# Kernel tuning notes

Measured on AMD Instinct MI355X. Metric: run time of the kernel, lower is better.

The kernel has to match this reference:

```python
import jax, jax.numpy as jnp
import numpy as np

B, S, DIM, HEADS, EXPERTS = 2, 2048, 1024, 16, 8
DFF = 4 * DIM
EPS = 1e-5


def setup_inputs() -> dict:
    key = jax.random.key(0)
    ks = jax.random.split(key, 16)
    w = lambda k, shp: jax.random.normal(k, shp, dtype=jnp.float32) * 0.02
    return {
        "x": jax.random.normal(ks[0], (B, S, DIM), dtype=jnp.float32),
        "ln1_g": jnp.ones((DIM,), jnp.float32), "ln1_b": jnp.zeros((DIM,), jnp.float32),
        "ln2_g": jnp.ones((DIM,), jnp.float32), "ln2_b": jnp.zeros((DIM,), jnp.float32),
        "wq": w(ks[1], (DIM, DIM)), "bq": jnp.zeros((DIM,), jnp.float32),
        "wk": w(ks[2], (DIM, DIM)), "bk": jnp.zeros((DIM,), jnp.float32),
        "wv": w(ks[3], (DIM, DIM)), "bv": jnp.zeros((DIM,), jnp.float32),
        "wo": w(ks[4], (DIM, DIM)), "bo": jnp.zeros((DIM,), jnp.float32),
        "w1": w(ks[5], (EXPERTS, DIM, DFF)), "b1": jnp.zeros((EXPERTS, DFF), jnp.float32),
        "w2": w(ks[6], (EXPERTS, DFF, DIM)), "b2": jnp.zeros((EXPERTS, DIM), jnp.float32),
        "token_split": np.full(EXPERTS, S // EXPERTS, dtype=np.int64),  # static split sizes
        "heads": HEADS,
    }


def _layernorm(h, g, b):
    m = h.mean(-1, keepdims=True)
    v = ((h - m) ** 2).mean(-1, keepdims=True)
    return (h - m) * jax.lax.rsqrt(v + EPS) * g + b


def reference(x, ln1_g, ln1_b, ln2_g, ln2_b, wq, bq, wk, bk, wv, bv, wo, bo,
              w1, b1, w2, b2, token_split, heads):
    Bx, Sx, D = x.shape
    Dh = D // heads
    # --- attention on norm1(x) ---
    h = _layernorm(x, ln1_g, ln1_b)
    q = (h @ wq + bq).reshape(Bx, Sx, heads, Dh)
    k = (h @ wk + bk).reshape(Bx, Sx, heads, Dh)
    v = (h @ wv + bv).reshape(Bx, Sx, heads, Dh)
    scores = jnp.einsum('bqhd,bkhd->bhqk', q, k) * (Dh ** -0.5)
    attn = jax.nn.softmax(scores, axis=-1)
    o = jnp.einsum('bhqk,bkhd->bqhd', attn, v).reshape(Bx, Sx, D)
    x = x + (o @ wo + bo)
    # --- token-chunked per-expert MLP ---
    residual = x
    h = _layernorm(x, ln2_g, ln2_b)
    split_pts = np.cumsum(np.asarray(token_split))[:-1]  # static boundaries
    chunks = jnp.split(h, split_pts, axis=1)
    outs = [jax.nn.silu(c @ w1[e] + b1[e]) @ w2[e] + b2[e]
            for e, c in enumerate(chunks)]
    return jnp.concatenate(outs, axis=1) + residual
```

## Files before the change

kernel.cpp:

```cpp
#include <hip/hip_runtime.h>


typedef unsigned int  u32;
typedef unsigned short u16;
typedef short v8s __attribute__((ext_vector_type(8)));
typedef float v4f __attribute__((ext_vector_type(4)));

#define SEQ  2048
#define DIM_ 1024
#define EPS_ 1e-5f

__device__ __forceinline__ u16 f2bf(float f) {
    __bf16 h = (__bf16)f;
    return __builtin_bit_cast(u16, h);
}

__device__ __forceinline__ void gload16(const void* g, void* l) {
    __builtin_amdgcn_global_load_lds((const __attribute__((address_space(1))) u32*)g,
                                     (__attribute__((address_space(3))) u32*)l, 16, 0, 0);
}

template<bool SEP>
__global__ __launch_bounds__(256) void conv_t(const float* __restrict__ s0,
                                              const float* __restrict__ s1,
                                              const float* __restrict__ s2,
                                              const float* __restrict__ s3,
                                              u16* __restrict__ dst, int K, int N) {
    __shared__ __attribute__((aligned(16))) u16 Ts[64][72];
    int tid = threadIdx.x;
    int z = blockIdx.z;
    const float* src = SEP ? (z == 0 ? s0 : z == 1 ? s1 : z == 2 ? s2 : s3)
                           : s0 + (size_t)z * K * N;
    u16* d = dst + (size_t)z * K * N;
    int k0 = blockIdx.y * 64, n0 = blockIdx.x * 64;
    int tk = tid >> 4, tn = tid & 15;

    u16 t[4][4];
    #pragma unroll
    for (int r = 0; r < 4; r++) {
        float4 L = *(const float4*)&src[(size_t)(k0 + tk * 4 + r) * N + n0 + tn * 4];
        t[r][0] = f2bf(L.x); t[r][1] = f2bf(L.y); t[r][2] = f2bf(L.z); t[r][3] = f2bf(L.w);
    }
    #pragma unroll
    for (int c = 0; c < 4; c++) {
        ushort4 q4 = { t[0][c], t[1][c], t[2][c], t[3][c] };
        *(ushort4*)&Ts[tn * 4 + c][tk * 4] = q4;
    }
    __syncthreads();
    #pragma unroll
    for (int i = 0; i < 2; i++) {
        int id = tid + i * 256;
        int row = id >> 3, ch = id & 7;
        v8s val = *(const v8s*)&Ts[row][ch * 8];
        *(v8s*)&d[(size_t)(n0 + row) * K + k0 + ch * 8] = val;
    }
}

__global__ __launch_bounds__(256) void ln_kernel(const float* __restrict__ x,
                                                 const float* __restrict__ g,
                                                 const float* __restrict__ b,
                                                 u16* __restrict__ out) {
    int row = blockIdx.x;
    int t = threadIdx.x;
    const float4* xr = (const float4*)(x + (size_t)row * DIM_);
    float4 v = xr[t];
    float s  = v.x + v.y + v.z + v.w;
    float ss = v.x*v.x + v.y*v.y + v.z*v.z + v.w*v.w;
    #pragma unroll
    for (int off = 32; off > 0; off >>= 1) {
        s  += __shfl_down(s, off);
        ss += __shfl_down(ss, off);
    }
    __shared__ float red[8];
    if ((t & 63) == 0) { red[t >> 6] = s; red[4 + (t >> 6)] = ss; }
    __syncthreads();
    s  = red[0] + red[1] + red[2] + red[3];
    ss = red[4] + red[5] + red[6] + red[7];
    float mean = s * (1.0f / DIM_);
    float var  = ss * (1.0f / DIM_) - mean * mean;
    float rstd = rsqrtf(var + EPS_);
    float4 gv = ((const float4*)g)[t];
    float4 bv = ((const float4*)b)[t];
    ushort4 ov;
    ov.x = f2bf((v.x - mean) * rstd * gv.x + bv.x);
    ov.y = f2bf((v.y - mean) * rstd * gv.y + bv.y);
    ov.z = f2bf((v.z - mean) * rstd * gv.z + bv.z);
    ov.w = f2bf((v.w - mean) * rstd * gv.w + bv.w);
    *(ushort4*)(out + (size_t)row * DIM_ + t * 4) = ov;
}

template<int BN, int ACT, bool GROUPED, int WMODE>
__global__ __launch_bounds__(256) void gemm_bf16(
    const u16* __restrict__ A, const u16* __restrict__ WT,
    const float* __restrict__ b0, const float* __restrict__ bk2, const float* __restrict__ bv2,
    const float* __restrict__ resid, float* __restrict__ Cf,
    u16* __restrict__ Cb, u16* __restrict__ Ckb, u16* __restrict__ vtb,
    int Nw, int K)
{
    constexpr int BM = 128;
    constexpr int MI = 4;
    constexpr int NI = BN / 32;
    __shared__ __attribute__((aligned(16))) char AsB[BM * 128];
    __shared__ __attribute__((aligned(16))) char BsB[BN * 128];

    int tid = threadIdx.x;
    int lane = tid & 63, w = tid >> 6;
    int wr = w >> 1, wc = w & 1;
    int g = lane >> 4, lq = lane & 15;

    long row0; int e = 0;
    const float* bias = b0;
    if (GROUPED) {
        int seg = blockIdx.y >> 1, mh = blockIdx.y & 1;
        int bb = seg >> 3; e = seg & 7;
        row0 = (long)bb * SEQ + e * 256 + mh * BM;
        bias += (size_t)e * Nw;
    } else row0 = (long)blockIdx.y * BM;

    int col0 = blockIdx.x * BN;
    int colL = col0;
    if (WMODE == 2) {
        int sel = col0 >> 10; colL = col0 & 1023;
        if (sel == 1)      bias = bk2;
        else if (sel == 2) bias = bv2;
    }

    const u16* Arow = A + (size_t)row0 * K;
    const u16* Brow = WT + (GROUPED ? ((size_t)e * Nw + col0) : (size_t)col0) * K;

    v4f acc[MI][NI];
    #pragma unroll
    for (int mi = 0; mi < MI; mi++)
        #pragma unroll
        for (int ni = 0; ni < NI; ni++) acc[mi][ni] = (v4f){0.f, 0.f, 0.f, 0.f};

    for (int kt = 0; kt < K; kt += 64) {
        #pragma unroll
        for (int i = 0; i < 4; i++) {
            int R0 = (i * 4 + w) * 8;
            int row = R0 + (lane >> 3);
            gload16(Arow + (size_t)row * K + kt + (((lane & 7) ^ (row & 7)) << 3),
                    AsB + R0 * 128);
        }
        #pragma unroll
        for (int i = 0; i < NI; i++) {
            int R0 = (i * 4 + w) * 8;
            int row = R0 + (lane >> 3);
            gload16(Brow + (size_t)row * K + kt + (((lane & 7) ^ (row & 7)) << 3),
                    BsB + R0 * 128);
        }
        __syncthreads();
        #pragma unroll
        for (int kk = 0; kk < 64; kk += 32) {
            v8s af[MI], bfv[NI];
            int slot = (kk >> 3) + g;
            #pragma unroll
            for (int mi = 0; mi < MI; mi++) {
                int row = wr * 64 + mi * 16 + lq;
                af[mi] = *(const v8s*)(AsB + row * 128 + ((slot ^ (row & 7)) << 4));
            }
            #pragma unroll
            for (int ni = 0; ni < NI; ni++) {
                int rn = wc * (BN / 2) + ni * 16 + lq;
                bfv[ni] = *(const v8s*)(BsB + rn * 128 + ((slot ^ (rn & 7)) << 4));
            }
            #pragma unroll
            for (int mi = 0; mi < MI; mi++)
                #pragma unroll
                for (int ni = 0; ni < NI; ni++)
                    acc[mi][ni] = __builtin_amdgcn_mfma_f32_16x16x32_bf16(
                        af[mi], bfv[ni], acc[mi][ni], 0, 0, 0);
        }
        __syncthreads();
    }

    #pragma unroll
    for (int mi = 0; mi < MI; mi++) {
        int grow = wr * 64 + mi * 16 + g * 4;
        #pragma unroll
        for (int ni = 0; ni < NI; ni++) {
            int cL = colL + wc * (BN / 2) + ni * 16 + lq;
            float bb_ = bias[cL];
            v4f a = acc[mi][ni];
            if (WMODE == 0) {
                #pragma unroll
                for (int r = 0; r < 4; r++) {
                    float val = a[r] + bb_;
                    if (ACT == 1) val = val / (1.0f + __expf(-val));
                    size_t idx = (size_t)(row0 + grow + r) * Nw + cL;
                    val += resid[idx];
                    Cf[idx] = val;
                }
            } else if (WMODE == 1) {
                #pragma unroll
                for (int r = 0; r < 4; r++) {
                    float val = a[r] + bb_;
                    if (ACT == 1) val = val / (1.0f + __expf(-val));
                    Cb[(size_t)(row0 + grow + r) * Nw + cL] = f2bf(val);
                }
            } else {
                int sel = col0 >> 10;
                if (sel < 2) {
                    u16* dst = (sel == 0) ? Cb : Ckb;
                    #pragma unroll
                    for (int r = 0; r < 4; r++)
                        dst[(size_t)(row0 + grow + r) * 1024 + cL] = f2bf(a[r] + bb_);
                } else {
                    long token0 = row0 + grow;
                    int bb2 = (int)(token0 >> 11);
                    int ss  = (int)(token0 & 2047);
                    int hh = cL >> 6, dd = cL & 63;
                    ushort4 pv_;
                    pv_.x = f2bf(a[0] + bb_); pv_.y = f2bf(a[1] + bb_);
                    pv_.z = f2bf(a[2] + bb_); pv_.w = f2bf(a[3] + bb_);
                    *(ushort4*)(vtb + ((size_t)(bb2 * 16 + hh) * 64 + dd) * 2048 + ss) = pv_;
                }
            }
        }
    }
}

__global__ __launch_bounds__(256) void attn_kernel(const u16* __restrict__ qb,
                                                   const u16* __restrict__ kb,
                                                   const u16* __restrict__ vtb,
                                                   u16* __restrict__ ob) {
    __shared__ __attribute__((aligned(16))) char Kl[8192];
    __shared__ __attribute__((aligned(16))) char Vl[8192];
    __shared__ __attribute__((aligned(16))) char Pl[4][4608];

    int tid = threadIdx.x;
    int lane = tid & 63, w = tid >> 6;
    int g = lane >> 4, lq = lane & 15;
    int h = blockIdx.y, bz = blockIdx.z;
    int q0 = blockIdx.x * 128 + w * 32;
    const size_t hb = (size_t)h * 64;

    v8s qfr[2][2];
    #pragma unroll
    for (int qi = 0; qi < 2; qi++)
        #pragma unroll
        for (int kkh = 0; kkh < 2; kkh++)
            qfr[qi][kkh] = *(const v8s*)(qb + ((size_t)(bz * SEQ + q0 + qi * 16 + lq)) * DIM_
                                         + hb + kkh * 32 + g * 8);

    v4f oacc[2][4];
    #pragma unroll
    for (int qi = 0; qi < 2; qi++)
        #pragma unroll
        for (int df = 0; df < 4; df++) oacc[qi][df] = (v4f){0.f, 0.f, 0.f, 0.f};
    float m_prev[2] = {-1e30f, -1e30f}, l_acc[2] = {0.f, 0.f};

    for (int kv = 0; kv < SEQ; kv += 64) {
        __syncthreads();
        #pragma unroll
        for (int i = 0; i < 2; i++) {
            int beta = (i * 4 + w) * 1024 + lane * 16;
            int row  = beta >> 7;
            int sc   = ((lane & 7) ^ (row & 7)) << 3;
            gload16(kb + ((size_t)(bz * SEQ + kv + row)) * DIM_ + hb + sc,
                    Kl + (i * 4 + w) * 1024);
            gload16(vtb + ((size_t)((bz * 16 + h) * 64 + row)) * 2048 + kv + sc,
                    Vl + (i * 4 + w) * 1024);
        }
        __syncthreads();

        v4f sa[4][2];
        #pragma unroll
        for (int cf = 0; cf < 4; cf++)
            #pragma unroll
            for (int qi = 0; qi < 2; qi++) sa[cf][qi] = (v4f){0.f, 0.f, 0.f, 0.f};
        #pragma unroll
        for (int kkh = 0; kkh < 2; kkh++) {
            v8s kf[4];
            int slot = kkh * 4 + g;
            #pragma unroll
            for (int cf = 0; cf < 4; cf++) {
                int row = cf * 16 + lq;
                kf[cf] = *(const v8s*)(Kl + row * 128 + ((slot ^ (row & 7)) << 4));
            }
            #pragma unroll
            for (int cf = 0; cf < 4; cf++)
                #pragma unroll
                for (int qi = 0; qi < 2; qi++)
                    sa[cf][qi] = __builtin_amdgcn_mfma_f32_16x16x32_bf16(
                        kf[cf], qfr[qi][kkh], sa[cf][qi], 0, 0, 0);
        }

        #pragma unroll
        for (int qi = 0; qi < 2; qi++) {
            float mx = -1e30f;
            #pragma unroll
            for (int cf = 0; cf < 4; cf++)
                #pragma unroll
                for (int r = 0; r < 4; r++) mx = fmaxf(mx, sa[cf][qi][r]);
            mx = fmaxf(mx, __shfl_xor(mx, 16));
            mx = fmaxf(mx, __shfl_xor(mx, 32));
            float rm = mx * 0.125f;
            if (__any(rm - m_prev[qi] > 8.0f)) {
                float mnew = fmaxf(m_prev[qi], rm);
                float corr = __expf(m_prev[qi] - mnew);
                m_prev[qi] = mnew;
                l_acc[qi] *= corr;
                #pragma unroll
                for (int r = 0; r < 4; r++) {
                    float cr = __shfl(corr, (lane & 48) | (g * 4 + r));
                    #pragma unroll
                    for (int df = 0; df < 4; df++) oacc[qi][df][r] *= cr;
                }
            }
            float rs = 0.f;
            float ps[4][4];
            #pragma unroll
            for (int cf = 0; cf < 4; cf++)
                #pragma unroll
                for (int r = 0; r < 4; r++) {
                    float p = __expf(sa[cf][qi][r] * 0.125f - m_prev[qi]);
                    ps[cf][r] = p; rs += p;
                }
            rs += __shfl_xor(rs, 16);
            rs += __shfl_xor(rs, 32);
            l_acc[qi] += rs;
            #pragma unroll
            for (int cf = 0; cf < 4; cf++) {
                ushort4 pw;
                pw.x = f2bf(ps[cf][0]); pw.y = f2bf(ps[cf][1]);
                pw.z = f2bf(ps[cf][2]); pw.w = f2bf(ps[cf][3]);
                *(ushort4*)(Pl[w] + (qi * 16 + lq) * 144 + (cf * 16 + g * 4) * 2) = pw;
            }
        }
        asm volatile("s_waitcnt lgkmcnt(0)" ::: "memory");
        __builtin_amdgcn_sched_barrier(0);

        #pragma unroll
        for (int kkh = 0; kkh < 2; kkh++) {
            v8s pa[2], vf[4];
            int slot = kkh * 4 + g;
            #pragma unroll
            for (int qi = 0; qi < 2; qi++)
                pa[qi] = *(const v8s*)(Pl[w] + (qi * 16 + lq) * 144 + kkh * 64 + g * 16);
            #pragma unroll
            for (int df = 0; df < 4; df++) {
                int row = df * 16 + lq;
                vf[df] = *(const v8s*)(Vl + row * 128 + ((slot ^ (row & 7)) << 4));
            }
            #pragma unroll
            for (int qi = 0; qi < 2; qi++)
                #pragma unroll
                for (int df = 0; df < 4; df++)
                    oacc[qi][df] = __builtin_amdgcn_mfma_f32_16x16x32_bf16(
                        pa[qi], vf[df], oacc[qi][df], 0, 0, 0);
        }
    }

    #pragma unroll
    for (int qi = 0; qi < 2; qi++) {
        float inv = 1.0f / l_acc[qi];
        #pragma unroll
        for (int r = 0; r < 4; r++) {
            float ivr = __shfl(inv, (lane & 48) | (g * 4 + r));
            size_t rowi = (size_t)(bz * SEQ + q0 + qi * 16 + g * 4 + r) * DIM_ + hb;
            #pragma unroll
            for (int df = 0; df < 4; df++)
                ob[rowi + df * 16 + lq] = f2bf(oacc[qi][df][r] * ivr);
        }
    }
}

extern "C" void kernel_launch(void* const* d_in, const int* in_sizes, int n_in,
                              void* d_out, int out_size, void* d_ws, size_t ws_size,
                              hipStream_t stream) {
    const float* x     = (const float*)d_in[0];
    const float* ln1_g = (const float*)d_in[1];
    const float* ln1_b = (const float*)d_in[2];
    const float* ln2_g = (const float*)d_in[3];
    const float* ln2_b = (const float*)d_in[4];
    const float* wq = (const float*)d_in[5];  const float* bq = (const float*)d_in[6];
    const float* wk = (const float*)d_in[7];  const float* bk = (const float*)d_in[8];
    const float* wv = (const float*)d_in[9];  const float* bv = (const float*)d_in[10];
    const float* wo = (const float*)d_in[11]; const float* bo = (const float*)d_in[12];
    const float* w1 = (const float*)d_in[13]; const float* b1 = (const float*)d_in[14];
    const float* w2 = (const float*)d_in[15]; const float* b2 = (const float*)d_in[16];

    char* wsb = (char*)d_ws;
    const size_t MB = 1024 * 1024;
    u16*   h1   = (u16*)(wsb + 0 * MB);
    u16*   qbf  = (u16*)(wsb + 8 * MB);
    u16*   kbf  = (u16*)(wsb + 16 * MB);
    u16*   vt   = (u16*)(wsb + 24 * MB);
    float* x2   = (float*)(wsb + 32 * MB);
    u16*   wqkvoT = (u16*)(wsb + 48 * MB);
    u16*   mid  = (u16*)(wsb + 48 * MB);
    u16*   w1T  = (u16*)(wsb + 80 * MB);
    u16*   w2T  = (u16*)(wsb + 80 * MB);
    u16*   ob   = h1;
    u16*   h2   = qbf;
    float* outp = (float*)d_out;

    conv_t<true ><<<dim3(16, 16, 4), 256, 0, stream>>>(wq, wk, wv, wo, wqkvoT, 1024, 1024);
    conv_t<false><<<dim3(64, 16, 8), 256, 0, stream>>>(w1, nullptr, nullptr, nullptr, w1T, 1024, 4096);

    ln_kernel<<<4096, 256, 0, stream>>>(x, ln1_g, ln1_b, h1);

    gemm_bf16<128, 0, false, 2><<<dim3(24, 32), 256, 0, stream>>>(
        h1, wqkvoT, bq, bk, bv, nullptr, nullptr, qbf, kbf, vt, 1024, 1024);

    attn_kernel<<<dim3(16, 16, 2), 256, 0, stream>>>(qbf, kbf, vt, ob);

    gemm_bf16<64, 0, false, 0><<<dim3(16, 32), 256, 0, stream>>>(
        ob, wqkvoT + (size_t)3 * 1024 * 1024, bo, nullptr, nullptr, x, x2,
        nullptr, nullptr, nullptr, 1024, 1024);

    ln_kernel<<<4096, 256, 0, stream>>>(x2, ln2_g, ln2_b, h2);

    gemm_bf16<128, 1, true, 1><<<dim3(32, 32), 256, 0, stream>>>(
        h2, w1T, b1, nullptr, nullptr, nullptr, nullptr,
        mid, nullptr, nullptr, 4096, 1024);

    conv_t<false><<<dim3(16, 64, 8), 256, 0, stream>>>(w2, nullptr, nullptr, nullptr, w2T, 4096, 1024);

    gemm_bf16<64, 0, true, 0><<<dim3(16, 32), 256, 0, stream>>>(
        mid, w2T, b2, nullptr, nullptr, x2, outp,
        nullptr, nullptr, nullptr, 1024, 4096);
}
```

Before: 596.9 us.

## Add double-buffered 256x256 GEMM kernel for QKV and FFN1 projections

Adds a new 512-thread GEMM kernel with 256x256 output tiles and two LDS buffers. It prefetches the next K-tiles through global_load_lds while computing the current one, using vmcnt waits and raised priority around the MFMAs. The QKV and W1 GEMMs now use this kernel, which cuts per-tile sync stalls and raises data reuse per loaded byte. In exchange, launch grids shrink to 192 and 256 blocks, and 128 KB of LDS per block limits occupancy.

```diff
diff --git a/kernel.cpp b/kernel.cpp
--- a/kernel.cpp
+++ b/kernel.cpp
@@ -89,117 +89,105 @@
     *(ushort4*)(out + (size_t)row * DIM_ + t * 4) = ov;
 }
 
-template<int BN, int ACT, bool GROUPED, int WMODE>
-__global__ __launch_bounds__(256) void gemm_bf16(
+template<int WMODE, bool GROUPED, int ACT>
+__global__ __launch_bounds__(512) void gemm2p(
     const u16* __restrict__ A, const u16* __restrict__ WT,
     const float* __restrict__ b0, const float* __restrict__ bk2, const float* __restrict__ bv2,
-    const float* __restrict__ resid, float* __restrict__ Cf,
     u16* __restrict__ Cb, u16* __restrict__ Ckb, u16* __restrict__ vtb,
     int Nw, int K)
 {
-    constexpr int BM = 128;
-    constexpr int MI = 4;
-    constexpr int NI = BN / 32;
-    __shared__ __attribute__((aligned(16))) char AsB[BM * 128];
-    __shared__ __attribute__((aligned(16))) char BsB[BN * 128];
+    __shared__ __attribute__((aligned(16))) char Ab[2][32768];
+    __shared__ __attribute__((aligned(16))) char Bb[2][32768];
 
     int tid = threadIdx.x;
     int lane = tid & 63, w = tid >> 6;
-    int wr = w >> 1, wc = w & 1;
+    int wm = w >> 2, wn = w & 3;
     int g = lane >> 4, lq = lane & 15;
 
     long row0; int e = 0;
     const float* bias = b0;
     if (GROUPED) {
-        int seg = blockIdx.y >> 1, mh = blockIdx.y & 1;
-        int bb = seg >> 3; e = seg & 7;
-        row0 = (long)bb * SEQ + e * 256 + mh * BM;
+        int bb = (int)blockIdx.y >> 3; e = blockIdx.y & 7;
+        row0 = (long)bb * SEQ + e * 256;
         bias += (size_t)e * Nw;
-    } else row0 = (long)blockIdx.y * BM;
-
-    int col0 = blockIdx.x * BN;
-    int colL = col0;
+    } else row0 = (long)blockIdx.y * 256;
+
+    int col0 = blockIdx.x * 256;
+    int colL = col0, sel = 0;
     if (WMODE == 2) {
-        int sel = col0 >> 10; colL = col0 & 1023;
-        if (sel == 1)      bias = bk2;
-        else if (sel == 2) bias = bv2;
+        sel = col0 >> 10; colL = col0 & 1023;
+        if (sel == 1) bias = bk2; else if (sel == 2) bias = bv2;
     }
 
     const u16* Arow = A + (size_t)row0 * K;
     const u16* Brow = WT + (GROUPED ? ((size_t)e * Nw + col0) : (size_t)col0) * K;
 
-    v4f acc[MI][NI];
-    #pragma unroll
-    for (int mi = 0; mi < MI; mi++)
-        #pragma unroll
-        for (int ni = 0; ni < NI; ni++) acc[mi][ni] = (v4f){0.f, 0.f, 0.f, 0.f};
-
-    for (int kt = 0; kt < K; kt += 64) {
+    v4f acc[8][4];
+    #pragma unroll
+    for (int mi = 0; mi < 8; mi++)
+        #pragma unroll
+        for (int ni = 0; ni < 4; ni++) acc[mi][ni] = (v4f){0.f, 0.f, 0.f, 0.f};
+
+    const int NT = K >> 6;
+
+    auto STAGE = [&](int tt, int p) {
+        int kb = tt * 64;
         #pragma unroll
         for (int i = 0; i < 4; i++) {
-            int R0 = (i * 4 + w) * 8;
+            int R0 = (i * 8 + w) * 8;
             int row = R0 + (lane >> 3);
-            gload16(Arow + (size_t)row * K + kt + (((lane & 7) ^ (row & 7)) << 3),
-                    AsB + R0 * 128);
-        }
-        #pragma unroll
-        for (int i = 0; i < NI; i++) {
-            int R0 = (i * 4 + w) * 8;
-            int row = R0 + (lane >> 3);
-            gload16(Brow + (size_t)row * K + kt + (((lane & 7) ^ (row & 7)) << 3),
-                    BsB + R0 * 128);
-        }
-        __syncthreads();
-        #pragma unroll
-        for (int kk = 0; kk < 64; kk += 32) {
-            v8s af[MI], bfv[NI];
-            int slot = (kk >> 3) + g;
-            #pragma unroll
-            for (int mi = 0; mi < MI; mi++) {
-                int row = wr * 64 + mi * 16 + lq;
-                af[mi] = *(const v8s*)(AsB + row * 128 + ((slot ^ (row & 7)) << 4));
-            }
-            #pragma unroll
-            for (int ni = 0; ni < NI; ni++) {
-                int rn = wc * (BN / 2) + ni * 16 + lq;
-                bfv[ni] = *(const v8s*)(BsB + rn * 128 + ((slot ^ (rn & 7)) << 4));
-            }
-            #pragma unroll
-            for (int mi = 0; mi < MI; mi++)
-                #pragma unroll
-                for (int ni = 0; ni < NI; ni++)
+            int sc = ((lane & 7) ^ (row & 7)) << 3;
+            gload16(Arow + (size_t)row * K + kb + sc, Ab[p] + R0 * 128);
+            gload16(Brow + (size_t)row * K + kb + sc, Bb[p] + R0 * 128);
+        }
+    };
+
+    STAGE(0, 0);
+    STAGE(1, 1);
+
+    for (int t = 0; t < NT; t++) {
+        int par = t & 1;
+        if (t < NT - 1) asm volatile("s_waitcnt vmcnt(8)" ::: "memory");
+        else            asm volatile("s_waitcnt vmcnt(0)" ::: "memory");
+        __builtin_amdgcn_s_barrier();
+        __builtin_amdgcn_sched_barrier(0);
+        #pragma unroll
+        for (int kh = 0; kh < 2; kh++) {
+            v8s af[8], bf[4];
+            int slot = kh * 4 + g;
+            #pragma unroll
+            for (int mi = 0; mi < 8; mi++) {
+                int row = wm * 128 + mi * 16 + lq;
+                af[mi] = *(const v8s*)(Ab[par] + row * 128 + ((slot ^ (row & 7)) << 4));
+            }
+            #pragma unroll
+            for (int ni = 0; ni < 4; ni++) {
+                int rn = wn * 64 + ni * 16 + lq;
+                bf[ni] = *(const v8s*)(Bb[par] + rn * 128 + ((slot ^ (rn & 7)) << 4));
+            }
+            __builtin_amdgcn_s_setprio(1);
+            #pragma unroll
+            for (int mi = 0; mi < 8; mi++)
+                #pragma unroll
+                for (int ni = 0; ni < 4; ni++)
                     acc[mi][ni] = __builtin_amdgcn_mfma_f32_16x16x32_bf16(
-                        af[mi], bfv[ni], acc[mi][ni], 0, 0, 0);
-        }
-        __syncthreads();
-    }
-
-    #pragma unroll
-    for (int mi = 0; mi < MI; mi++) {
-        int grow = wr * 64 + mi * 16 + g * 4;
-        #pragma unroll
-        for (int ni = 0; ni < NI; ni++) {
-            int cL = colL + wc * (BN / 2) + ni * 16 + lq;
+                        af[mi], bf[ni], acc[mi][ni], 0, 0, 0);
+            __builtin_amdgcn_s_setprio(0);
+        }
+        __builtin_amdgcn_sched_barrier(0);
+        __builtin_amdgcn_s_barrier();
+        if (t + 2 < NT) STAGE(t + 2, par);
+    }
+
+    #pragma unroll
+    for (int mi = 0; mi < 8; mi++) {
+        int grow = wm * 128 + mi * 16 + g * 4;
+        #pragma unroll
+        for (int ni = 0; ni < 4; ni++) {
+            int cL = colL + wn * 64 + ni * 16 + lq;
             float bb_ = bias[cL];
             v4f a = acc[mi][ni];
-            if (WMODE == 0) {
-                #pragma unroll
-                for (int r = 0; r < 4; r++) {
-                    float val = a[r] + bb_;
-                    if (ACT == 1) val = val / (1.0f + __expf(-val));
-                    size_t idx = (size_t)(row0 + grow + r) * Nw + cL;
-                    val += resid[idx];
-                    Cf[idx] = val;
-                }
-            } else if (WMODE == 1) {
-                #pragma unroll
-                for (int r = 0; r < 4; r++) {
-                    float val = a[r] + bb_;
-                    if (ACT == 1) val = val / (1.0f + __expf(-val));
-                    Cb[(size_t)(row0 + grow + r) * Nw + cL] = f2bf(val);
-                }
-            } else {
-                int sel = col0 >> 10;
+            if (WMODE == 2) {
                 if (sel < 2) {
                     u16* dst = (sel == 0) ? Cb : Ckb;
                     #pragma unroll
@@ -215,6 +203,107 @@
                     pv_.z = f2bf(a[2] + bb_); pv_.w = f2bf(a[3] + bb_);
                     *(ushort4*)(vtb + ((size_t)(bb2 * 16 + hh) * 64 + dd) * 2048 + ss) = pv_;
                 }
+            } else {
+                #pragma unroll
+                for (int r = 0; r < 4; r++) {
+                    float val = a[r] + bb_;
+                    if (ACT == 1) val = val / (1.0f + __expf(-val));
+                    Cb[(size_t)(row0 + grow + r) * Nw + cL] = f2bf(val);
+                }
+            }
+        }
+    }
+}
+
+template<int BN, bool GROUPED>
+__global__ __launch_bounds__(256) void gemm_bf16(
+    const u16* __restrict__ A, const u16* __restrict__ WT,
+    const float* __restrict__ b0,
+    const float* __restrict__ resid, float* __restrict__ Cf,
+    int Nw, int K)
+{
+    constexpr int BM = 128;
+    constexpr int MI = 4;
+    constexpr int NI = BN / 32;
+    __shared__ __attribute__((aligned(16))) char AsB[BM * 128];
+    __shared__ __attribute__((aligned(16))) char BsB[BN * 128];
+
+    int tid = threadIdx.x;
+    int lane = tid & 63, w = tid >> 6;
+    int wr = w >> 1, wc = w & 1;
+    int g = lane >> 4, lq = lane & 15;
+
+    long row0; int e = 0;
+    const float* bias = b0;
+    if (GROUPED) {
+        int seg = blockIdx.y >> 1, mh = blockIdx.y & 1;
+        int bb = seg >> 3; e = seg & 7;
+        row0 = (long)bb * SEQ + e * 256 + mh * BM;
+        bias += (size_t)e * Nw;
+    } else row0 = (long)blockIdx.y * BM;
+
+    int col0 = blockIdx.x * BN;
+    const u16* Arow = A + (size_t)row0 * K;
+    const u16* Brow = WT + (GROUPED ? ((size_t)e * Nw + col0) : (size_t)col0) * K;
+
+    v4f acc[MI][NI];
+    #pragma unroll
+    for (int mi = 0; mi < MI; mi++)
+        #pragma unroll
+        for (int ni = 0; ni < NI; ni++) acc[mi][ni] = (v4f){0.f, 0.f, 0.f, 0.f};
+
+    for (int kt = 0; kt < K; kt += 64) {
+        #pragma unroll
+        for (int i = 0; i < 4; i++) {
+            int R0 = (i * 4 + w) * 8;
+            int row = R0 + (lane >> 3);
+            gload16(Arow + (size_t)row * K + kt + (((lane & 7) ^ (row & 7)) << 3),
+                    AsB + R0 * 128);
+        }
+        #pragma unroll
+        for (int i = 0; i < NI; i++) {
+            int R0 = (i * 4 + w) * 8;
+            int row = R0 + (lane >> 3);
+            gload16(Brow + (size_t)row * K + kt + (((lane & 7) ^ (row & 7)) << 3),
+                    BsB + R0 * 128);
+        }
+        __syncthreads();
+        #pragma unroll
+        for (int kk = 0; kk < 64; kk += 32) {
+            v8s af[MI], bfv[NI];
+            int slot = (kk >> 3) + g;
+            #pragma unroll
+            for (int mi = 0; mi < MI; mi++) {
+                int row = wr * 64 + mi * 16 + lq;
+                af[mi] = *(const v8s*)(AsB + row * 128 + ((slot ^ (row & 7)) << 4));
+            }
+            #pragma unroll
+            for (int ni = 0; ni < NI; ni++) {
+                int rn = wc * (BN / 2) + ni * 16 + lq;
+                bfv[ni] = *(const v8s*)(BsB + rn * 128 + ((slot ^ (rn & 7)) << 4));
+            }
+            #pragma unroll
+            for (int mi = 0; mi < MI; mi++)
+                #pragma unroll
+                for (int ni = 0; ni < NI; ni++)
+                    acc[mi][ni] = __builtin_amdgcn_mfma_f32_16x16x32_bf16(
+                        af[mi], bfv[ni], acc[mi][ni], 0, 0, 0);
+        }
+        __syncthreads();
+    }
+
+    #pragma unroll
+    for (int mi = 0; mi < MI; mi++) {
+        int grow = wr * 64 + mi * 16 + g * 4;
+        #pragma unroll
+        for (int ni = 0; ni < NI; ni++) {
+            int cL = col0 + wc * (BN / 2) + ni * 16 + lq;
+            float bb_ = bias[cL];
+            v4f a = acc[mi][ni];
+            #pragma unroll
+            for (int r = 0; r < 4; r++) {
+                size_t idx = (size_t)(row0 + grow + r) * Nw + cL;
+                Cf[idx] = a[r] + bb_ + resid[idx];
             }
         }
     }
@@ -401,24 +490,21 @@
 
     ln_kernel<<<4096, 256, 0, stream>>>(x, ln1_g, ln1_b, h1);
 
-    gemm_bf16<128, 0, false, 2><<<dim3(24, 32), 256, 0, stream>>>(
-        h1, wqkvoT, bq, bk, bv, nullptr, nullptr, qbf, kbf, vt, 1024, 1024);
+    gemm2p<2, false, 0><<<dim3(12, 16), 512, 0, stream>>>(
+        h1, wqkvoT, bq, bk, bv, qbf, kbf, vt, 1024, 1024);
 
     attn_kernel<<<dim3(16, 16, 2), 256, 0, stream>>>(qbf, kbf, vt, ob);
 
-    gemm_bf16<64, 0, false, 0><<<dim3(16, 32), 256, 0, stream>>>(
-        ob, wqkvoT + (size_t)3 * 1024 * 1024, bo, nullptr, nullptr, x, x2,
-        nullptr, nullptr, nullptr, 1024, 1024);
+    gemm_bf16<64, false><<<dim3(16, 32), 256, 0, stream>>>(
+        ob, wqkvoT + (size_t)3 * 1024 * 1024, bo, x, x2, 1024, 1024);
 
     ln_kernel<<<4096, 256, 0, stream>>>(x2, ln2_g, ln2_b, h2);
 
-    gemm_bf16<128, 1, true, 1><<<dim3(32, 32), 256, 0, stream>>>(
-        h2, w1T, b1, nullptr, nullptr, nullptr, nullptr,
-        mid, nullptr, nullptr, 4096, 1024);
+    gemm2p<1, true, 1><<<dim3(16, 16), 512, 0, stream>>>(
+        h2, w1T, b1, nullptr, nullptr, mid, nullptr, nullptr, 4096, 1024);
 
     conv_t<false><<<dim3(16, 64, 8), 256, 0, stream>>>(w2, nullptr, nullptr, nullptr, w2T, 4096, 1024);
 
-    gemm_bf16<64, 0, true, 0><<<dim3(16, 32), 256, 0, stream>>>(
-        mid, w2T, b2, nullptr, nullptr, x2, outp,
-        nullptr, nullptr, nullptr, 1024, 4096);
-}
+    gemm_bf16<64, true><<<dim3(16, 32), 256, 0, stream>>>(
+        mid, w2T, b2, x2, outp, 1024, 4096);
+}
```

Result: no change. 599.6 us (+0.5%).
